# Kernel optimization log

Measured on AMD Instinct MI355X. Metric: run time of the kernel, lower is better.

The kernel has to match this reference:

```python
import jax, jax.numpy as jnp
import numpy as np
import math

B, S, E, H, L, FF = 32, 512, 256, 8, 4, 1024
DH = E // H
EPS = 1e-5


def layernorm(x):
    # nn.LayerNorm(elementwise_affine=False)
    m = jnp.mean(x, axis=-1, keepdims=True)
    v = jnp.mean((x - m) ** 2, axis=-1, keepdims=True)
    return (x - m) / jnp.sqrt(v + EPS)


def make_pos_embedding(e):
    vals = [math.sin(1 / 10000 ** ((i - 1) / e)) if i % 2 == 1
            else math.cos(i / 10000 ** ((i - 1) / e)) for i in range(e)]
    return jnp.asarray(np.array(vals, dtype=np.float32))


def setup_inputs() -> dict:
    key = jax.random.key(0)
    ks = jax.random.split(key, 8)
    sc = 0.02
    x = jax.random.normal(ks[0], (B, S, E), dtype=jnp.float32)
    Wq = jax.random.normal(ks[1], (L, H, DH, DH), dtype=jnp.float32) * sc
    Wk = jax.random.normal(ks[2], (L, H, DH, DH), dtype=jnp.float32) * sc
    Wv = jax.random.normal(ks[3], (L, H, DH, DH), dtype=jnp.float32) * sc
    W1 = jax.random.normal(ks[4], (L, E, FF), dtype=jnp.float32) * sc
    b1 = jnp.zeros((L, FF), dtype=jnp.float32)
    W2 = jax.random.normal(ks[5], (L, FF, E), dtype=jnp.float32) * sc
    b2 = jnp.zeros((L, E), dtype=jnp.float32)
    pos = make_pos_embedding(E)
    return {"x": x, "pos": pos, "Wq": Wq, "Wk": Wk, "Wv": Wv,
            "W1": W1, "b1": b1, "W2": W2, "b2": b2}


def encoder_layer(x, wq, wk, wv, w1, bb1, w2, bb2):
    xn = layernorm(x)
    xh = xn.reshape(B, S, H, DH)  # split embedding into per-head chunks
    q = jnp.einsum('bshd,hde->bhse', xh, wq)
    k = jnp.einsum('bshd,hde->bhse', xh, wk)
    v = jnp.einsum('bshd,hde->bhse', xh, wv)
    scores = jnp.einsum('bhsd,bhtd->bhst', q, k) / jnp.sqrt(jnp.float32(DH))
    a = jax.nn.softmax(scores, axis=-1)
    o = jnp.einsum('bhst,bhtd->bhsd', a, v)
    mha = o.transpose(0, 2, 1, 3).reshape(B, S, E)  # concat heads
    res = mha + x
    rn = layernorm(res)
    ffn = jax.nn.gelu(rn @ w1 + bb1, approximate=False) @ w2 + bb2
    return ffn + res


def reference(x, pos, Wq, Wk, Wv, W1, b1, W2, b2):
    h = x + pos  # fixed sinusoidal positional embedding
    for l in range(L):
        h = encoder_layer(h, Wq[l], Wk[l], Wv[l], W1[l], b1[l], W2[l], b2[l])
    return h
```

## Files before the change

### kernel.cpp

```cpp
#include <hip/hip_runtime.h>
#include <math.h>

#define BB   32
#define SS   512
#define EE   256
#define HH   8
#define LL   4
#define FFD  1024
#define DHD  32

constexpr float LN_EPS = 1e-5f;
constexpr int   NBSE   = BB * SS * EE;

typedef float  f32x4  __attribute__((ext_vector_type(4)));
typedef __bf16 bf16;
typedef __bf16 bf16x4 __attribute__((ext_vector_type(4)));
typedef __bf16 bf16x8 __attribute__((ext_vector_type(8)));

#define WAITV(n) asm volatile("s_waitcnt vmcnt(" #n ")" ::: "memory")

__device__ __forceinline__ void glds16(const bf16* g, bf16* l) {
    __builtin_amdgcn_global_load_lds(
        (const __attribute__((address_space(1))) void*)g,
        (__attribute__((address_space(3))) void*)l,
        16, 0, 0);
}

__device__ __forceinline__ float gelu_f(float x) {
    float u = x * x;
    float t = 1.5957691216057308f * x * (1.0f + 0.044715f * u);
    return x / (1.0f + __expf(-t));
}

__global__ __launch_bounds__(256) void k_prep(const float* __restrict__ W1,
                                              const float* __restrict__ W2,
                                              const float* __restrict__ Wq,
                                              const float* __restrict__ Wk,
                                              const float* __restrict__ Wv,
                                              bf16* __restrict__ W1t,
                                              bf16* __restrict__ W2t,
                                              bf16* __restrict__ Wqt,
                                              bf16* __restrict__ Wkt,
                                              bf16* __restrict__ Wvt) {
    __shared__ float tile[32][33];
    int bid = blockIdx.x;
    int tx = threadIdx.x & 31, ty = threadIdx.x >> 5;
    if (bid < 2048) {
        bool isw2 = bid >= 1024;
        int id = isw2 ? bid - 1024 : bid;
        int K = isw2 ? FFD : EE, N = isw2 ? EE : FFD;
        int l = id >> 8, rem = id & 255;
        int n0, k0;
        if (isw2) { n0 = (rem & 7) * 32;  k0 = (rem >> 3) * 32; }
        else      { n0 = (rem & 31) * 32; k0 = (rem >> 5) * 32; }
        const float* in = (isw2 ? W2 : W1) + (size_t)l * K * N;
        bf16* out       = (isw2 ? W2t : W1t) + (size_t)l * K * N;
        #pragma unroll
        for (int i = 0; i < 32; i += 8)
            tile[ty + i][tx] = in[(size_t)(k0 + ty + i) * N + n0 + tx];
        __syncthreads();
        #pragma unroll
        for (int i = 0; i < 32; i += 8)
            out[(size_t)(n0 + ty + i) * K + k0 + tx] = (bf16)tile[tx][ty + i];
    } else {
        int id = bid - 2048;
        int lh = id & 31, z = id >> 5;
        const float* in = (z == 0 ? Wq : z == 1 ? Wk : Wv) + (size_t)lh * 1024;
        bf16* out       = (z == 0 ? Wqt : z == 1 ? Wkt : Wvt) + (size_t)lh * 1024;
        float scale = (z == 0) ? 0.17677669529663687f : 1.0f;
        #pragma unroll
        for (int i = 0; i < 32; i += 8)
            tile[ty + i][tx] = in[(ty + i) * 32 + tx];
        __syncthreads();
        #pragma unroll
        for (int i = 0; i < 32; i += 8)
            out[(ty + i) * 32 + tx] = (bf16)(tile[tx][ty + i] * scale);
    }
}

template <bool ADDPOS>
__global__ __launch_bounds__(256) void k_lnqkv(const float* __restrict__ xin,
                                               const float* __restrict__ pos,
                                               float* __restrict__ hout,
                                               const bf16* __restrict__ Wqt,
                                               const bf16* __restrict__ Wkt,
                                               const bf16* __restrict__ Wvt,
                                               bf16* __restrict__ qb,
                                               bf16* __restrict__ kb,
                                               bf16* __restrict__ vb) {
    __shared__ __attribute__((aligned(16))) bf16 Xs[32 * 264];
    int b = blockIdx.x, s0 = blockIdx.y * 32;
    int tid = threadIdx.x, w = tid >> 6, lane = tid & 63;
    size_t rowoff = ((size_t)(b * SS + s0 + w * 8)) * EE + lane * 4;
    const float* hb = xin + rowoff;
    float4 pv;
    if (ADDPOS) pv = *(const float4*)(pos + lane * 4);
    float4 xr[8];
    #pragma unroll
    for (int i = 0; i < 8; i++)
        xr[i] = *(const float4*)(hb + (size_t)i * EE);
    if (ADDPOS) {
        #pragma unroll
        for (int i = 0; i < 8; i++) {
            xr[i].x += pv.x; xr[i].y += pv.y; xr[i].z += pv.z; xr[i].w += pv.w;
            *(float4*)(hout + rowoff + (size_t)i * EE) = xr[i];
        }
    }
    #pragma unroll
    for (int i = 0; i < 8; i++) {
        float4 v4 = xr[i];
        float sum = v4.x + v4.y + v4.z + v4.w;
        #pragma unroll
        for (int m = 1; m <= 32; m <<= 1) sum += __shfl_xor(sum, m, 64);
        float mean = sum * (1.0f / EE);
        float dx = v4.x - mean, dy = v4.y - mean, dz = v4.z - mean, dw = v4.w - mean;
        float ss = dx * dx + dy * dy + dz * dz + dw * dw;
        #pragma unroll
        for (int m = 1; m <= 32; m <<= 1) ss += __shfl_xor(ss, m, 64);
        float rstd = rsqrtf(ss * (1.0f / EE) + LN_EPS);
        bf16x4 o4 = { (bf16)(dx * rstd), (bf16)(dy * rstd), (bf16)(dz * rstd), (bf16)(dw * rstd) };
        *(bf16x4*)&Xs[(w * 8 + i) * 264 + lane * 4] = o4;
    }
    __syncthreads();
    int col = lane & 15, quad = lane >> 4;
    int rt = w & 1, hgrp = w >> 1;
    #pragma unroll
    for (int hh2 = 0; hh2 < 4; hh2++) {
        int h = hgrp * 4 + hh2;
        bf16x8 a = *(const bf16x8*)&Xs[(rt * 16 + col) * 264 + h * 32 + quad * 8];
        size_t base = ((size_t)((b * HH + h) * SS) + s0 + rt * 16) * DHD;
        #pragma unroll
        for (int nt = 0; nt < 2; nt++) {
            int e = nt * 16 + col;
            bf16x8 bq  = *(const bf16x8*)(Wqt + (h * 32 + e) * 32 + quad * 8);
            bf16x8 bk2 = *(const bf16x8*)(Wkt + (h * 32 + e) * 32 + quad * 8);
            bf16x8 bv2 = *(const bf16x8*)(Wvt + (h * 32 + e) * 32 + quad * 8);
            f32x4 z = {0.f, 0.f, 0.f, 0.f};
            f32x4 cq = __builtin_amdgcn_mfma_f32_16x16x32_bf16(bq, a, z, 0, 0, 0);
            f32x4 ck = __builtin_amdgcn_mfma_f32_16x16x32_bf16(bk2, a, z, 0, 0, 0);
            f32x4 cv = __builtin_amdgcn_mfma_f32_16x16x32_bf16(a, bv2, z, 0, 0, 0);
            bf16x4 q4 = { (bf16)cq[0], (bf16)cq[1], (bf16)cq[2], (bf16)cq[3] };
            bf16x4 k4 = { (bf16)ck[0], (bf16)ck[1], (bf16)ck[2], (bf16)ck[3] };
            size_t tb = base + (size_t)col * DHD + nt * 16 + quad * 4;
            *(bf16x4*)&qb[tb] = q4;
            *(bf16x4*)&kb[tb] = k4;
            bf16x4 vv = { (bf16)cv[0], (bf16)cv[1], (bf16)cv[2], (bf16)cv[3] };
            *(bf16x4*)&vb[(((size_t)(b * HH + h)) * DHD + e) * SS + s0 + rt * 16 + quad * 4] = vv;
        }
    }
}

#define ATT_LDK 40
#define ATT_LDV 264
#define ATT_LDP 36
__global__ __launch_bounds__(256) void k_attn(const bf16* __restrict__ Q,
                                              const bf16* __restrict__ K,
                                              const bf16* __restrict__ VT,
                                              bf16* __restrict__ O) {
    __shared__ __attribute__((aligned(16))) bf16 Ks[256 * ATT_LDK];
    __shared__ __attribute__((aligned(16))) bf16 Vs[32 * ATT_LDV];
    __shared__ __attribute__((aligned(16))) bf16 Ps[4][16 * ATT_LDP];
    int bh = blockIdx.x;
    int q0 = blockIdx.y * 128;
    int tid = threadIdx.x;
    int w = tid >> 6, lane = tid & 63;
    int col = lane & 15, quad = lane >> 4;
    bf16x8 aq[2];
    #pragma unroll
    for (int sub = 0; sub < 2; sub++)
        aq[sub] = *(const bf16x8*)(Q + ((size_t)(bh * SS + q0 + sub * 64 + w * 16 + col)) * DHD + quad * 8);
    float lr[2] = {0.f, 0.f};
    f32x4 oacc[2][2] = {};
    int ksr = tid >> 2, ksc = (tid & 3) * 8;
    int vd  = tid >> 5, vso = (tid & 31) * 8;
    bf16x8 kr[4], vr[4];
    #pragma unroll
    for (int it = 0; it < 4; it++) {
        kr[it] = *(const bf16x8*)(K + ((size_t)(bh * SS + it * 64 + ksr)) * DHD + ksc);
        vr[it] = *(const bf16x8*)(VT + (((size_t)bh * DHD + it * 8 + vd) * SS) + vso);
    }
    for (int ph = 0; ph < 2; ph++) {
        __syncthreads();
        #pragma unroll
        for (int it = 0; it < 4; it++) {
            *(bf16x8*)&Ks[(it * 64 + ksr) * ATT_LDK + ksc] = kr[it];
            *(bf16x8*)&Vs[(it * 8 + vd) * ATT_LDV + vso] = vr[it];
        }
        if (ph == 0) {
            #pragma unroll
            for (int it = 0; it < 4; it++) {
                kr[it] = *(const bf16x8*)(K + ((size_t)(bh * SS + 256 + it * 64 + ksr)) * DHD + ksc);
                vr[it] = *(const bf16x8*)(VT + (((size_t)bh * DHD + it * 8 + vd) * SS) + 256 + vso);
            }
        }
        __syncthreads();
        #pragma unroll
        for (int i = 0; i < 8; i++) {
            bf16x8 bk[2], bv[2];
            #pragma unroll
            for (int nt = 0; nt < 2; nt++) {
                bk[nt] = *(const bf16x8*)&Ks[(i * 32 + nt * 16 + col) * ATT_LDK + quad * 8];
                bv[nt] = *(const bf16x8*)&Vs[(nt * 16 + col) * ATT_LDV + i * 32 + quad * 8];
            }
            __builtin_amdgcn_s_setprio(1);
            #pragma unroll
            for (int sub = 0; sub < 2; sub++) {
                #pragma unroll
                for (int nt = 0; nt < 2; nt++) {
                    f32x4 z = {0.f, 0.f, 0.f, 0.f};
                    f32x4 st = __builtin_amdgcn_mfma_f32_16x16x32_bf16(bk[nt], aq[sub], z, 0, 0, 0);
                    bf16x4 p4;
                    #pragma unroll
                    for (int r = 0; r < 4; r++) {
                        float p = __expf(st[r]);
                        lr[sub] += p;
                        p4[r] = (bf16)p;
                    }
                    *(bf16x4*)&Ps[w][col * ATT_LDP + nt * 16 + quad * 4] = p4;
                }
                bf16x4 apl = *(const bf16x4*)&Ps[w][col * ATT_LDP + quad * 8];
                bf16x4 aph = *(const bf16x4*)&Ps[w][col * ATT_LDP + quad * 8 + 4];
                bf16x8 ap;
                ap[0] = apl[0]; ap[1] = apl[1]; ap[2] = apl[2]; ap[3] = apl[3];
                ap[4] = aph[0]; ap[5] = aph[1]; ap[6] = aph[2]; ap[7] = aph[3];
                #pragma unroll
                for (int nt = 0; nt < 2; nt++)
                    oacc[sub][nt] = __builtin_amdgcn_mfma_f32_16x16x32_bf16(ap, bv[nt], oacc[sub][nt], 0, 0, 0);
            }
            __builtin_amdgcn_s_setprio(0);
        }
    }
    int b = bh >> 3, hh = bh & 7;
    #pragma unroll
    for (int sub = 0; sub < 2; sub++) {
        float ls = lr[sub];
        ls += __shfl_xor(ls, 16, 64);
        ls += __shfl_xor(ls, 32, 64);
        #pragma unroll
        for (int r = 0; r < 4; r++) {
            float lrow = __shfl(ls, quad * 4 + r, 64);
            float inv = 1.0f / lrow;
            int row = q0 + sub * 64 + w * 16 + quad * 4 + r;
            size_t ob = ((size_t)(b * SS + row)) * EE + hh * 32;
            O[ob + col]      = (bf16)(oacc[sub][0][r] * inv);
            O[ob + 16 + col] = (bf16)(oacc[sub][1][r] * inv);
        }
    }
}

__global__ __launch_bounds__(512) void k_ffn(const bf16* __restrict__ ob,
                                             const float* __restrict__ hb,
                                             const bf16* __restrict__ W1t_l,
                                             const float* __restrict__ b1_l,
                                             const bf16* __restrict__ W2t_l,
                                             const float* __restrict__ b2_l,
                                             float* __restrict__ Cf) {
    __shared__ __attribute__((aligned(16))) bf16 As[64 * 256];
    __shared__ __attribute__((aligned(16))) bf16 Gs[64 * 128];
    __shared__ __attribute__((aligned(16))) bf16 Bst[2][16384];
    __shared__ __attribute__((aligned(16))) float b1s[FFD];
    int tid = threadIdx.x, w = tid >> 6, lane = tid & 63;
    int col = lane & 15, quad = lane >> 4;
    int rg = w >> 2, cg = w & 3;
    int row0 = blockIdx.x * 64;

    *(float2*)&b1s[tid * 2] = *(const float2*)&b1_l[tid * 2];

    #pragma unroll 2
    for (int rr = 0; rr < 8; rr++) {
        int r = w * 8 + rr;
        size_t g = (size_t)(row0 + r) * EE + lane * 4;
        float4 h4 = *(const float4*)(hb + g);
        bf16x4 o4 = *(const bf16x4*)(ob + g);
        float v0 = h4.x + (float)o4[0], v1 = h4.y + (float)o4[1];
        float v2 = h4.z + (float)o4[2], v3 = h4.w + (float)o4[3];
        float s1 = v0 + v1 + v2 + v3;
        float s2 = v0 * v0 + v1 * v1 + v2 * v2 + v3 * v3;
        #pragma unroll
        for (int m = 1; m <= 32; m <<= 1) {
            s1 += __shfl_xor(s1, m, 64);
            s2 += __shfl_xor(s2, m, 64);
        }
        float mean = s1 * (1.0f / EE);
        float rstd = rsqrtf(s2 * (1.0f / EE) - mean * mean + LN_EPS);
        bf16x4 a4 = { (bf16)((v0 - mean) * rstd), (bf16)((v1 - mean) * rstd),
                      (bf16)((v2 - mean) * rstd), (bf16)((v3 - mean) * rstd) };
        *(bf16x4*)&As[r * 256 + ((lane * 4) ^ ((r & 7) << 3))] = a4;
    }
    asm volatile("s_waitcnt lgkmcnt(0)" ::: "memory");
    __builtin_amdgcn_s_barrier();
    asm volatile("s_waitcnt vmcnt(0)" ::: "memory");

    int srow = lane >> 3, spos = lane & 7;
    auto stageB1 = [&](int ch, int p, int slot) {
        #pragma unroll
        for (int i = 0; i < 2; i++) {
            int r = i * 64 + w * 8 + srow;
            glds16(W1t_l + (size_t)(ch * 128 + r) * EE + p * 64 + ((spos ^ (r & 7)) * 8),
                   &Bst[slot][i * 4096 + w * 512]);
        }
    };
    auto stageB2 = [&](int ch, int j, int slot) {
        #pragma unroll
        for (int i = 0; i < 4; i++) {
            int r = i * 64 + w * 8 + srow;
            glds16(W2t_l + (size_t)r * FFD + ch * 128 + j * 64 + ((spos ^ (r & 7)) * 8),
                   &Bst[slot][i * 4096 + w * 512]);
        }
    };

    f32x4 accO[2][4] = {};
    f32x4 accG[2][2] = {};
    stageB1(0, 0, 0);
    for (int ch = 0; ch < 8; ch++) {
        #pragma unroll
        for (int p = 0; p < 4; p++) {
            if (p < 3) { stageB1(ch, p + 1, (p + 1) & 1); WAITV(2); }
            else       { stageB2(ch, 0, 0);               WAITV(4); }
            __builtin_amdgcn_s_barrier();
            bf16x8 af[2][2], bfr[2][2];
            #pragma unroll
            for (int mt = 0; mt < 2; mt++) {
                int r = rg * 32 + mt * 16 + col;
                #pragma unroll
                for (int kk = 0; kk < 2; kk++)
                    af[mt][kk] = *(const bf16x8*)&As[r * 256 + ((p * 64 + kk * 32 + quad * 8) ^ ((r & 7) << 3))];
            }
            #pragma unroll
            for (int nt = 0; nt < 2; nt++) {
                int c = cg * 32 + nt * 16 + col;
                #pragma unroll
                for (int kk = 0; kk < 2; kk++)
                    bfr[nt][kk] = *(const bf16x8*)&Bst[p & 1][c * 64 + ((kk * 32 + quad * 8) ^ ((c & 7) << 3))];
            }
            #pragma unroll
            for (int kk = 0; kk < 2; kk++)
                #pragma unroll
                for (int mt = 0; mt < 2; mt++)
                    #pragma unroll
                    for (int nt = 0; nt < 2; nt++)
                        accG[mt][nt] = __builtin_amdgcn_mfma_f32_16x16x32_bf16(bfr[nt][kk], af[mt][kk], accG[mt][nt], 0, 0, 0);
            if (p == 3) {
                #pragma unroll
                for (int mt = 0; mt < 2; mt++) {
                    int t = rg * 32 + mt * 16 + col;
                    #pragma unroll
                    for (int nt = 0; nt < 2; nt++) {
                        int f = cg * 32 + nt * 16 + quad * 4;
                        float4 b4 = *(const float4*)&b1s[ch * 128 + f];
                        bf16x4 g4;
                        g4[0] = (bf16)gelu_f(accG[mt][nt][0] + b4.x);
                        g4[1] = (bf16)gelu_f(accG[mt][nt][1] + b4.y);
                        g4[2] = (bf16)gelu_f(accG[mt][nt][2] + b4.z);
                        g4[3] = (bf16)gelu_f(accG[mt][nt][3] + b4.w);
                        *(bf16x4*)&Gs[t * 128 + (f ^ ((t & 7) << 3))] = g4;
                        f32x4 z = {0.f, 0.f, 0.f, 0.f};
                        accG[mt][nt] = z;
                    }
                }
                asm volatile("s_waitcnt lgkmcnt(0)" ::: "memory");
            }
            __builtin_amdgcn_s_barrier();
        }
        #pragma unroll
        for (int j = 0; j < 2; j++) {
            if (j == 0)      { stageB2(ch, 1, 1);     WAITV(4); }
            else if (ch < 7) { stageB1(ch + 1, 0, 0); WAITV(2); }
            else             { WAITV(0); }
            __builtin_amdgcn_s_barrier();
            bf16x8 af2[2][2], bf2[4][2];
            #pragma unroll
            for (int mt = 0; mt < 2; mt++) {
                int r = rg * 32 + mt * 16 + col;
                #pragma unroll
                for (int kk = 0; kk < 2; kk++)
                    af2[mt][kk] = *(const bf16x8*)&Gs[r * 128 + ((j * 64 + kk * 32 + quad * 8) ^ ((r & 7) << 3))];
            }
            #pragma unroll
            for (int nt = 0; nt < 4; nt++) {
                int c = cg * 64 + nt * 16 + col;
                #pragma unroll
                for (int kk = 0; kk < 2; kk++)
                    bf2[nt][kk] = *(const bf16x8*)&Bst[j & 1][c * 64 + ((kk * 32 + quad * 8) ^ ((c & 7) << 3))];
            }
            #pragma unroll
            for (int kk = 0; kk < 2; kk++)
                #pragma unroll
                for (int mt = 0; mt < 2; mt++)
                    #pragma unroll
                    for (int nt = 0; nt < 4; nt++)
                        accO[mt][nt] = __builtin_amdgcn_mfma_f32_16x16x32_bf16(bf2[nt][kk], af2[mt][kk], accO[mt][nt], 0, 0, 0);
            __builtin_amdgcn_s_barrier();
        }
    }
    #pragma unroll
    for (int mt = 0; mt < 2; mt++) {
        int row = row0 + rg * 32 + mt * 16 + col;
        #pragma unroll
        for (int nt = 0; nt < 4; nt++) {
            int cc = cg * 64 + nt * 16 + quad * 4;
            float4 b4 = *(const float4*)&b2_l[cc];
            float4 h4 = *(const float4*)&hb[(size_t)row * EE + cc];
            bf16x4 o4 = *(const bf16x4*)&ob[(size_t)row * EE + cc];
            float4 out;
            out.x = accO[mt][nt][0] + b4.x + h4.x + (float)o4[0];
            out.y = accO[mt][nt][1] + b4.y + h4.y + (float)o4[1];
            out.z = accO[mt][nt][2] + b4.z + h4.z + (float)o4[2];
            out.w = accO[mt][nt][3] + b4.w + h4.w + (float)o4[3];
            *(float4*)&Cf[(size_t)row * EE + cc] = out;
        }
    }
}

extern "C" void kernel_launch(void* const* d_in, const int* in_sizes, int n_in,
                              void* d_out, int out_size, void* d_ws, size_t ws_size,
                              hipStream_t stream) {
    (void)in_sizes; (void)n_in; (void)out_size; (void)ws_size;
    const float* x   = (const float*)d_in[0];
    const float* pos = (const float*)d_in[1];
    const float* Wq  = (const float*)d_in[2];
    const float* Wk  = (const float*)d_in[3];
    const float* Wv  = (const float*)d_in[4];
    const float* W1  = (const float*)d_in[5];
    const float* b1  = (const float*)d_in[6];
    const float* W2  = (const float*)d_in[7];
    const float* b2  = (const float*)d_in[8];

    float* ws = (float*)d_ws;
    size_t N = (size_t)NBSE;
    float* h  = ws;
    bf16* ob  = (bf16*)(ws + N);
    bf16* qb  = (bf16*)(ws + 2 * N);
    bf16* kb  = qb + N;
    bf16* vb  = kb + N;
    bf16* W1t = (bf16*)(ws + 4 * N);
    bf16* W2t = W1t + (size_t)LL * EE * FFD;
    bf16* Wqt = W2t + (size_t)LL * EE * FFD;
    bf16* Wkt = Wqt + (size_t)LL * HH * DHD * DHD;
    bf16* Wvt = Wkt + (size_t)LL * HH * DHD * DHD;

    k_prep<<<2144, 256, 0, stream>>>(W1, W2, Wq, Wk, Wv, W1t, W2t, Wqt, Wkt, Wvt);
    for (int l = 0; l < LL; l++) {
        if (l == 0)
            k_lnqkv<true><<<dim3(BB, SS / 32), 256, 0, stream>>>(
                x, pos, h, Wqt, Wkt, Wvt, qb, kb, vb);
        else
            k_lnqkv<false><<<dim3(BB, SS / 32), 256, 0, stream>>>(
                h, nullptr, nullptr,
                Wqt + (size_t)l * HH * DHD * DHD, Wkt + (size_t)l * HH * DHD * DHD,
                Wvt + (size_t)l * HH * DHD * DHD, qb, kb, vb);
        k_attn<<<dim3(BB * HH, SS / 128), 256, 0, stream>>>(qb, kb, vb, ob);
        float* outp = (l == LL - 1) ? (float*)d_out : h;
        k_ffn<<<BB * SS / 64, 512, 0, stream>>>(
            ob, h, W1t + (size_t)l * FFD * EE, b1 + (size_t)l * FFD,
            W2t + (size_t)l * EE * FFD, b2 + (size_t)l * EE, outp);
    }
}
```

Baseline: 393.3 us.

## Load FFN weights directly from global into registers instead of LDS staging

The fused FFN kernel no longer double-buffers W1/W2 tiles through shared memory with async global-to-LDS copies and per-step barriers. Each wave now reads its MFMA B fragments straight from global memory (relying on L2 and cache reuse), and synchronises only around the GELU intermediate in LDS. Dropping the 64 KB staging buffer cuts LDS use and adds a launch-bounds hint for more resident blocks. The cost is more global and L2 traffic, since the same weights are reread by every wave that shares them, and load latency now has to be hidden by occupancy.

```diff
diff --git a/kernel.cpp b/kernel.cpp
--- a/kernel.cpp
+++ b/kernel.cpp
@@ -16,15 +16,6 @@
 typedef __bf16 bf16;
 typedef __bf16 bf16x4 __attribute__((ext_vector_type(4)));
 typedef __bf16 bf16x8 __attribute__((ext_vector_type(8)));
-
-#define WAITV(n) asm volatile("s_waitcnt vmcnt(" #n ")" ::: "memory")
-
-__device__ __forceinline__ void glds16(const bf16* g, bf16* l) {
-    __builtin_amdgcn_global_load_lds(
-        (const __attribute__((address_space(1))) void*)g,
-        (__attribute__((address_space(3))) void*)l,
-        16, 0, 0);
-}
 
 __device__ __forceinline__ float gelu_f(float x) {
     float u = x * x;
@@ -248,16 +239,15 @@
     }
 }
 
-__global__ __launch_bounds__(512) void k_ffn(const bf16* __restrict__ ob,
-                                             const float* __restrict__ hb,
-                                             const bf16* __restrict__ W1t_l,
-                                             const float* __restrict__ b1_l,
-                                             const bf16* __restrict__ W2t_l,
-                                             const float* __restrict__ b2_l,
-                                             float* __restrict__ Cf) {
+__global__ __launch_bounds__(512, 4) void k_ffn(const bf16* __restrict__ ob,
+                                                const float* __restrict__ hb,
+                                                const bf16* __restrict__ W1t_l,
+                                                const float* __restrict__ b1_l,
+                                                const bf16* __restrict__ W2t_l,
+                                                const float* __restrict__ b2_l,
+                                                float* __restrict__ Cf) {
     __shared__ __attribute__((aligned(16))) bf16 As[64 * 256];
     __shared__ __attribute__((aligned(16))) bf16 Gs[64 * 128];
-    __shared__ __attribute__((aligned(16))) bf16 Bst[2][16384];
     __shared__ __attribute__((aligned(16))) float b1s[FFD];
     int tid = threadIdx.x, w = tid >> 6, lane = tid & 63;
     int col = lane & 15, quad = lane >> 4;
@@ -287,111 +277,71 @@
                       (bf16)((v2 - mean) * rstd), (bf16)((v3 - mean) * rstd) };
         *(bf16x4*)&As[r * 256 + ((lane * 4) ^ ((r & 7) << 3))] = a4;
     }
-    asm volatile("s_waitcnt lgkmcnt(0)" ::: "memory");
-    __builtin_amdgcn_s_barrier();
-    asm volatile("s_waitcnt vmcnt(0)" ::: "memory");
-
-    int srow = lane >> 3, spos = lane & 7;
-    auto stageB1 = [&](int ch, int p, int slot) {
-        #pragma unroll
-        for (int i = 0; i < 2; i++) {
-            int r = i * 64 + w * 8 + srow;
-            glds16(W1t_l + (size_t)(ch * 128 + r) * EE + p * 64 + ((spos ^ (r & 7)) * 8),
-                   &Bst[slot][i * 4096 + w * 512]);
-        }
-    };
-    auto stageB2 = [&](int ch, int j, int slot) {
-        #pragma unroll
-        for (int i = 0; i < 4; i++) {
-            int r = i * 64 + w * 8 + srow;
-            glds16(W2t_l + (size_t)r * FFD + ch * 128 + j * 64 + ((spos ^ (r & 7)) * 8),
-                   &Bst[slot][i * 4096 + w * 512]);
-        }
-    };
+    __syncthreads();
 
     f32x4 accO[2][4] = {};
-    f32x4 accG[2][2] = {};
-    stageB1(0, 0, 0);
+    const bf16* W1p = W1t_l + (size_t)(cg * 32 + col) * EE + quad * 8;
+    const bf16* W2p = W2t_l + (size_t)(cg * 64 + col) * FFD + quad * 8;
+
     for (int ch = 0; ch < 8; ch++) {
-        #pragma unroll
-        for (int p = 0; p < 4; p++) {
-            if (p < 3) { stageB1(ch, p + 1, (p + 1) & 1); WAITV(2); }
-            else       { stageB2(ch, 0, 0);               WAITV(4); }
-            __builtin_amdgcn_s_barrier();
-            bf16x8 af[2][2], bfr[2][2];
+        f32x4 accG[2][2] = {};
+        #pragma unroll
+        for (int ks = 0; ks < 8; ks++) {
+            bf16x8 bfr[2], af[2];
+            #pragma unroll
+            for (int nt = 0; nt < 2; nt++)
+                bfr[nt] = *(const bf16x8*)(W1p + (size_t)(ch * 128 + nt * 16) * EE + ks * 32);
             #pragma unroll
             for (int mt = 0; mt < 2; mt++) {
                 int r = rg * 32 + mt * 16 + col;
+                af[mt] = *(const bf16x8*)&As[r * 256 + ((ks * 32 + quad * 8) ^ ((r & 7) << 3))];
+            }
+            #pragma unroll
+            for (int mt = 0; mt < 2; mt++)
                 #pragma unroll
-                for (int kk = 0; kk < 2; kk++)
-                    af[mt][kk] = *(const bf16x8*)&As[r * 256 + ((p * 64 + kk * 32 + quad * 8) ^ ((r & 7) << 3))];
-            }
+                for (int nt = 0; nt < 2; nt++)
+                    accG[mt][nt] = __builtin_amdgcn_mfma_f32_16x16x32_bf16(bfr[nt], af[mt], accG[mt][nt], 0, 0, 0);
+        }
+        #pragma unroll
+        for (int mt = 0; mt < 2; mt++) {
+            int t = rg * 32 + mt * 16 + col;
             #pragma unroll
             for (int nt = 0; nt < 2; nt++) {
-                int c = cg * 32 + nt * 16 + col;
-                #pragma unroll
-                for (int kk = 0; kk < 2; kk++)
-                    bfr[nt][kk] = *(const bf16x8*)&Bst[p & 1][c * 64 + ((kk * 32 + quad * 8) ^ ((c & 7) << 3))];
-            }
-            #pragma unroll
-            for (int kk = 0; kk < 2; kk++)
-                #pragma unroll
-                for (int mt = 0; mt < 2; mt++)
-                    #pragma unroll
-                    for (int nt = 0; nt < 2; nt++)
-                        accG[mt][nt] = __builtin_amdgcn_mfma_f32_16x16x32_bf16(bfr[nt][kk], af[mt][kk], accG[mt][nt], 0, 0, 0);
-            if (p == 3) {
-                #pragma unroll
-                for (int mt = 0; mt < 2; mt++) {
-                    int t = rg * 32 + mt * 16 + col;
-                    #pragma unroll
-                    for (int nt = 0; nt < 2; nt++) {
-                        int f = cg * 32 + nt * 16 + quad * 4;
-                        float4 b4 = *(const float4*)&b1s[ch * 128 + f];
-                        bf16x4 g4;
-                        g4[0] = (bf16)gelu_f(accG[mt][nt][0] + b4.x);
-                        g4[1] = (bf16)gelu_f(accG[mt][nt][1] + b4.y);
-                        g4[2] = (bf16)gelu_f(accG[mt][nt][2] + b4.z);
-                        g4[3] = (bf16)gelu_f(accG[mt][nt][3] + b4.w);
-                        *(bf16x4*)&Gs[t * 128 + (f ^ ((t & 7) << 3))] = g4;
-                        f32x4 z = {0.f, 0.f, 0.f, 0.f};
-                        accG[mt][nt] = z;
-                    }
-                }
-                asm volatile("s_waitcnt lgkmcnt(0)" ::: "memory");
-            }
-            __builtin_amdgcn_s_barrier();
-        }
-        #pragma unroll
-        for (int j = 0; j < 2; j++) {
-            if (j == 0)      { stageB2(ch, 1, 1);     WAITV(4); }
-            else if (ch < 7) { stageB1(ch + 1, 0, 0); WAITV(2); }
-            else             { WAITV(0); }
-            __builtin_amdgcn_s_barrier();
-            bf16x8 af2[2][2], bf2[4][2];
+                int f = cg * 32 + nt * 16 + quad * 4;
+                float4 b4 = *(const float4*)&b1s[ch * 128 + f];
+                bf16x4 g4;
+                g4[0] = (bf16)gelu_f(accG[mt][nt][0] + b4.x);
+                g4[1] = (bf16)gelu_f(accG[mt][nt][1] + b4.y);
+                g4[2] = (bf16)gelu_f(accG[mt][nt][2] + b4.z);
+                g4[3] = (bf16)gelu_f(accG[mt][nt][3] + b4.w);
+                *(bf16x4*)&Gs[t * 128 + (f ^ ((t & 7) << 3))] = g4;
+            }
+        }
+        bf16x8 bf2p[4];
+        #pragma unroll
+        for (int nt = 0; nt < 4; nt++)
+            bf2p[nt] = *(const bf16x8*)(W2p + (size_t)(nt * 16) * FFD + ch * 128);
+        asm volatile("s_waitcnt lgkmcnt(0)" ::: "memory");
+        __builtin_amdgcn_s_barrier();
+        #pragma unroll
+        for (int fs = 0; fs < 4; fs++) {
+            bf16x8 bf2[4], af2[2];
+            #pragma unroll
+            for (int nt = 0; nt < 4; nt++)
+                bf2[nt] = (fs == 0) ? bf2p[nt]
+                        : *(const bf16x8*)(W2p + (size_t)(nt * 16) * FFD + ch * 128 + fs * 32);
             #pragma unroll
             for (int mt = 0; mt < 2; mt++) {
                 int r = rg * 32 + mt * 16 + col;
+                af2[mt] = *(const bf16x8*)&Gs[r * 128 + ((fs * 32 + quad * 8) ^ ((r & 7) << 3))];
+            }
+            #pragma unroll
+            for (int mt = 0; mt < 2; mt++)
                 #pragma unroll
-                for (int kk = 0; kk < 2; kk++)
-                    af2[mt][kk] = *(const bf16x8*)&Gs[r * 128 + ((j * 64 + kk * 32 + quad * 8) ^ ((r & 7) << 3))];
-            }
-            #pragma unroll
-            for (int nt = 0; nt < 4; nt++) {
-                int c = cg * 64 + nt * 16 + col;
-                #pragma unroll
-                for (int kk = 0; kk < 2; kk++)
-                    bf2[nt][kk] = *(const bf16x8*)&Bst[j & 1][c * 64 + ((kk * 32 + quad * 8) ^ ((c & 7) << 3))];
-            }
-            #pragma unroll
-            for (int kk = 0; kk < 2; kk++)
-                #pragma unroll
-                for (int mt = 0; mt < 2; mt++)
-                    #pragma unroll
-                    for (int nt = 0; nt < 4; nt++)
-                        accO[mt][nt] = __builtin_amdgcn_mfma_f32_16x16x32_bf16(bf2[nt][kk], af2[mt][kk], accO[mt][nt], 0, 0, 0);
-            __builtin_amdgcn_s_barrier();
-        }
+                for (int nt = 0; nt < 4; nt++)
+                    accO[mt][nt] = __builtin_amdgcn_mfma_f32_16x16x32_bf16(bf2[nt], af2[mt], accO[mt][nt], 0, 0, 0);
+        }
+        __builtin_amdgcn_s_barrier();
     }
     #pragma unroll
     for (int mt = 0; mt < 2; mt++) {
```

New measurement: 525.0 us. 33.5% more time.
